# Optimization experiments

Measured on AMD Instinct MI355X. Metric: run time of the kernel, lower is better.

## Reference

```python
import jax, jax.numpy as jnp
import numpy as np

N_NODES = 50000
ALPHA_SLOPE = 0.2  # LeakyReLU negative slope
EPS = 1e-16


def setup_inputs() -> dict:
    key = jax.random.key(0)
    k1, k2, k3, k4 = jax.random.split(key, 4)
    in_features, heads, d = 512, 8, 32
    x = jax.random.normal(k1, (N_NODES, in_features), dtype=jnp.float32)
    edge_index = jax.random.randint(k2, (2, 800000), 0, N_NODES, dtype=jnp.int64)
    # xavier_normal with relu gain ~ sqrt(2) * sqrt(2/(fan_in+fan_out))
    w_std = np.sqrt(2.0) * np.sqrt(2.0 / (in_features + d))
    a_std = np.sqrt(2.0) * np.sqrt(2.0 / (1 + 2 * d))
    W = jax.random.normal(k3, (heads, in_features, d), dtype=jnp.float32) * w_std
    a = jax.random.normal(k4, (heads, 2 * d), dtype=jnp.float32) * a_std
    return {"x": x, "edge_index": edge_index, "W": W, "a": a}


def reference(x, edge_index, W, a):
    # x: [N, F_in], edge_index: [2, E], W: [H, F_in, D], a: [H, 2D]
    n = x.shape[0]
    d = W.shape[-1]
    e0, e1 = edge_index[0], edge_index[1]
    # per-head projected features: [N, H, D]
    h = jnp.einsum('nf,hfd->nhd', x, W)
    # attention logits: a.mm(cat(h[e0], h[e1]).T) == a_src.h[e0] + a_dst.h[e1]
    a_src, a_dst = a[:, :d], a[:, d:]          # [H, D] each
    s_src = jnp.einsum('nhd,hd->nh', h, a_src)  # [N, H]
    s_dst = jnp.einsum('nhd,hd->nh', h, a_dst)  # [N, H]
    logits = s_src[e0] + s_dst[e1]              # [E, H]
    logits = jnp.where(logits >= 0, logits, ALPHA_SLOPE * logits)  # LeakyReLU
    # segment softmax over destination node e0
    m = jax.ops.segment_max(logits, e0, num_segments=n)   # [N, H]
    ex = jnp.exp(logits - m[e0])                          # [E, H]
    denom = jax.ops.segment_sum(ex, e0, num_segments=n)   # [N, H]
    alpha = ex / (denom[e0] + EPS)                        # [E, H]
    # dropout is identity in eval mode
    # sparse aggregate: out[e0] += alpha * h[e1]
    msg = alpha[:, :, None] * h[e1]                       # [E, H, D]
    out = jax.ops.segment_sum(msg, e0, num_segments=n)    # [N, H, D]
    return out.reshape(n, -1)                             # concat heads -> [N, H*D]
```

## Files before the change

### kernel.cpp

```cpp
#include <hip/hip_runtime.h>
#include <hip/hip_bf16.h>

#define N_NODES 50000
#define N_EDGES 800000
#define IN_F    512
#define HEADS   8
#define DHEAD   32
#define NHD     256
#define SLOPE   0.2f
#define EPS_F   1e-16f
#define N_SBLK  ((N_NODES + 255) / 256)
#define NB_GEMM ((N_NODES + 63) / 64)
#define NB_HIST ((N_EDGES + 4095) / 4096)

typedef __attribute__((ext_vector_type(8))) short short8;
typedef __attribute__((ext_vector_type(4))) float f32x4;
typedef __attribute__((ext_vector_type(4))) unsigned short u16x4;
typedef __attribute__((ext_vector_type(4))) unsigned int u32x4;

__device__ __forceinline__ unsigned short f2bf(float f) {
  unsigned int u = __float_as_uint(f);
  unsigned int r = u + 0x7FFFu + ((u >> 16) & 1u);
  return (unsigned short)(r >> 16);
}
__device__ __forceinline__ float bf2f(unsigned short s) {
  return __uint_as_float(((unsigned int)s) << 16);
}
__device__ __forceinline__ unsigned int pkbf(float a, float b) {
  __hip_bfloat162 t = __float22bfloat162_rn(float2{a, b});
  unsigned int r;
  __builtin_memcpy(&r, &t, sizeof(r));
  return r;
}
__device__ __forceinline__ void gload_lds16(const void* g, void* l) {
  __builtin_amdgcn_global_load_lds((const __attribute__((address_space(1))) void*)g,
                                   (__attribute__((address_space(3))) void*)l, 16, 0, 0);
}

__global__ void k_cast_w(const float* __restrict__ W, unsigned short* __restrict__ WbT,
                         int* __restrict__ deg) {
  int id = blockIdx.x * blockDim.x + threadIdx.x;
  if (id < NHD * IN_F) {
    int c = id >> 9, k = id & 511;
    WbT[id] = f2bf(W[(c >> 5) * (IN_F * DHEAD) + k * DHEAD + (c & 31)]);
  }
  if (id < N_NODES) deg[id] = 0;
}

__global__ __launch_bounds__(256) void k_gemm_mfma(const float* __restrict__ x,
                                                   const unsigned short* __restrict__ WbT,
                                                   unsigned short* __restrict__ hb,
                                                   const float* __restrict__ a,
                                                   float* __restrict__ s_src,
                                                   float* __restrict__ s_dst,
                                                   const int* __restrict__ ei,
                                                   int* __restrict__ deg) {
  if (blockIdx.x >= NB_GEMM) {
    int b = blockIdx.x - NB_GEMM;
    int end = min(b * 4096 + 4096, N_EDGES);
    for (int e = b * 4096 + threadIdx.x; e < end; e += 256)
      atomicAdd(&deg[ei[e]], 1);
    return;
  }

  __shared__ unsigned short As[64 * 32];
  __shared__ unsigned short Bs[256 * 32];
  const int tid  = threadIdx.x;
  const int lane = tid & 63;
  const int wid  = tid >> 6;
  const int bm   = blockIdx.x * 64;
  const int wn   = wid * 64;

  const int arow = tid >> 2, ap = tid & 3, aq = ap ^ ((arow >> 1) & 3);
  const float* gA = x + (size_t)min(bm + arow, N_NODES - 1) * IN_F + aq * 8;
  unsigned short* lA = &As[(arow * 4 + ap) * 8];

  const int brow0 = 64 * wid + (lane >> 2);
  const int bq = (lane & 3) ^ ((lane >> 3) & 3);
  const unsigned short* gB0 = WbT + (size_t)brow0 * IN_F + bq * 8;
  unsigned short* lBw = &Bs[((size_t)256 * wid + lane) * 8];

  f32x4 acc[4][4] = {};

#pragma unroll
  for (int t = 0; t < 16; ++t) {
    const int k0 = t * 32;
    __syncthreads();
#pragma unroll
    for (int it = 0; it < 4; ++it)
      gload_lds16(gB0 + k0 + it * 16 * IN_F, lBw + it * 64 * 8);
    {
      float4 lo = *(const float4*)(gA + k0);
      float4 hi = *(const float4*)(gA + k0 + 4);
      u32x4 v = { pkbf(lo.x, lo.y), pkbf(lo.z, lo.w),
                  pkbf(hi.x, hi.y), pkbf(hi.z, hi.w) };
      *(u32x4*)lA = v;
    }
    __syncthreads();

    const int dl = lane & 15;
    const int p  = (lane >> 4) ^ ((dl >> 1) & 3);
    short8 af[4], bfr[4];
#pragma unroll
    for (int i = 0; i < 4; ++i)
      af[i] = *(const short8*)&As[((i * 16 + dl) * 4 + p) * 8];
#pragma unroll
    for (int j = 0; j < 4; ++j)
      bfr[j] = *(const short8*)&Bs[((wn + j * 16 + dl) * 4 + p) * 8];
#pragma unroll
    for (int i = 0; i < 4; ++i)
#pragma unroll
      for (int j = 0; j < 4; ++j)
        acc[i][j] = __builtin_amdgcn_mfma_f32_16x16x32_bf16(af[i], bfr[j], acc[i][j], 0, 0, 0);
  }

  const int h0 = 2 * wid, h1 = 2 * wid + 1;
  const int dl = lane & 15;
  const float as00 = a[h0 * 64 + dl],      as01 = a[h0 * 64 + 16 + dl];
  const float as10 = a[h1 * 64 + dl],      as11 = a[h1 * 64 + 16 + dl];
  const float ad00 = a[h0 * 64 + 32 + dl], ad01 = a[h0 * 64 + 48 + dl];
  const float ad10 = a[h1 * 64 + 32 + dl], ad11 = a[h1 * 64 + 48 + dl];

#pragma unroll
  for (int i = 0; i < 4; ++i) {
#pragma unroll
    for (int q = 0; q < 4; ++q) {
      int row = bm + i * 16 + (lane >> 4) * 4 + q;
      float ss0 = acc[i][0][q] * as00 + acc[i][1][q] * as01;
      float ss1 = acc[i][2][q] * as10 + acc[i][3][q] * as11;
      float sd0 = acc[i][0][q] * ad00 + acc[i][1][q] * ad01;
      float sd1 = acc[i][2][q] * ad10 + acc[i][3][q] * ad11;
#pragma unroll
      for (int o = 1; o < 16; o <<= 1) {
        ss0 += __shfl_xor(ss0, o);
        ss1 += __shfl_xor(ss1, o);
        sd0 += __shfl_xor(sd0, o);
        sd1 += __shfl_xor(sd1, o);
      }
      if (row < N_NODES) {
#pragma unroll
        for (int j = 0; j < 4; ++j)
          hb[(size_t)row * NHD + wn + j * 16 + dl] = f2bf(acc[i][j][q]);
        if (dl == 0) {
          s_src[row * 8 + h0] = ss0;
          s_src[row * 8 + h1] = ss1;
          s_dst[row * 8 + h0] = sd0;
          s_dst[row * 8 + h1] = sd1;
        }
      }
    }
  }
}

__global__ __launch_bounds__(256) void k_bsum(const int* __restrict__ deg,
                                              int* __restrict__ bsum) {
  __shared__ int sm[4];
  int i = blockIdx.x * 256 + threadIdx.x;
  int v = (i < N_NODES) ? deg[i] : 0;
#pragma unroll
  for (int o = 1; o < 64; o <<= 1) v += __shfl_xor(v, o);
  if ((threadIdx.x & 63) == 0) sm[threadIdx.x >> 6] = v;
  __syncthreads();
  if (threadIdx.x == 0) bsum[blockIdx.x] = sm[0] + sm[1] + sm[2] + sm[3];
}

__global__ __launch_bounds__(256) void k_scan_main(const int* __restrict__ deg,
                                                   const int* __restrict__ bsum,
                                                   int* __restrict__ rowptr,
                                                   int* __restrict__ cursor) {
  __shared__ int sb[256];
  __shared__ int sm[256];
  const int t = threadIdx.x;
  const int b = blockIdx.x;
  int bv = (t < N_SBLK) ? bsum[t] : 0;
  sb[t] = bv;
  int i = b * 256 + t;
  int v = (i < N_NODES) ? deg[i] : 0;
  sm[t] = v;
  __syncthreads();
#pragma unroll
  for (int o = 1; o < 256; o <<= 1) {
    int u1 = (t >= o) ? sb[t - o] : 0;
    int u2 = (t >= o) ? sm[t - o] : 0;
    __syncthreads();
    sb[t] += u1;
    sm[t] += u2;
    __syncthreads();
  }
  int boff = (b > 0) ? sb[b - 1] : 0;
  if (i < N_NODES) {
    int ex = boff + sm[t] - v;
    rowptr[i] = ex;
    cursor[i] = ex;
  }
  if (b == 0 && t == 0) rowptr[N_NODES] = sb[255];
}

__global__ void k_fill(const int* __restrict__ ei, int* __restrict__ cursor,
                       int* __restrict__ edst) {
  int e = blockIdx.x * blockDim.x + threadIdx.x;
  if (e >= N_EDGES) return;
  int p = atomicAdd(&cursor[ei[e]], 1);
  edst[p] = ei[N_EDGES + e];
}

__global__ __launch_bounds__(256) void k_aggr(const int* __restrict__ rowptr,
                                              const int* __restrict__ edst,
                                              const float* __restrict__ s_src,
                                              const float* __restrict__ s_dst,
                                              const unsigned short* __restrict__ hb,
                                              float* __restrict__ out) {
  int n = (int)((blockIdx.x * blockDim.x + threadIdx.x) >> 6);
  if (n >= N_NODES) return;
  n = __builtin_amdgcn_readfirstlane(n);
  const int lane = threadIdx.x & 63;
  const int head = lane >> 3;
  const float ssrc = s_src[n * 8 + head];
  int i = rowptr[n];
  const int iend = rowptr[n + 1];
  float den = 0.f;
  f32x4 acc = {0.f, 0.f, 0.f, 0.f};
  for (; i + 1 < iend; i += 2) {
    int d0 = edst[i], d1 = edst[i + 1];
    float v0 = ssrc + s_dst[d0 * 8 + head];
    float v1 = ssrc + s_dst[d1 * 8 + head];
    u16x4 h0 = *(const u16x4*)(hb + (size_t)d0 * NHD + lane * 4);
    u16x4 h1 = *(const u16x4*)(hb + (size_t)d1 * NHD + lane * 4);
    v0 = v0 >= 0.f ? v0 : SLOPE * v0;
    v1 = v1 >= 0.f ? v1 : SLOPE * v1;
    float e0 = __expf(v0), e1 = __expf(v1);
    den += e0 + e1;
    acc.x += e0 * bf2f(h0.x) + e1 * bf2f(h1.x);
    acc.y += e0 * bf2f(h0.y) + e1 * bf2f(h1.y);
    acc.z += e0 * bf2f(h0.z) + e1 * bf2f(h1.z);
    acc.w += e0 * bf2f(h0.w) + e1 * bf2f(h1.w);
  }
  if (i < iend) {
    int d0 = edst[i];
    float v0 = ssrc + s_dst[d0 * 8 + head];
    v0 = v0 >= 0.f ? v0 : SLOPE * v0;
    float e0 = __expf(v0);
    u16x4 h0 = *(const u16x4*)(hb + (size_t)d0 * NHD + lane * 4);
    den += e0;
    acc.x += e0 * bf2f(h0.x);
    acc.y += e0 * bf2f(h0.y);
    acc.z += e0 * bf2f(h0.z);
    acc.w += e0 * bf2f(h0.w);
  }
  float inv = 1.f / (den + EPS_F);
  *(f32x4*)(out + (size_t)n * NHD + lane * 4) = acc * inv;
}

extern "C" void kernel_launch(void* const* d_in, const int* in_sizes, int n_in,
                              void* d_out, int out_size, void* d_ws, size_t ws_size,
                              hipStream_t stream) {
  const float* x  = (const float*)d_in[0];
  const int*   ei = (const int*)d_in[1];
  const float* W  = (const float*)d_in[2];
  const float* a  = (const float*)d_in[3];
  float* out = (float*)d_out;

  unsigned short* hb  = (unsigned short*)d_ws;
  unsigned short* WbT = hb + (size_t)N_NODES * NHD;
  float* s_src = (float*)(WbT + (size_t)NHD * IN_F);
  float* s_dst = s_src + (size_t)N_NODES * HEADS;
  int* deg    = (int*)(s_dst + (size_t)N_NODES * HEADS);
  int* cursor = deg + N_NODES;
  int* rowptr = cursor + N_NODES;
  int* bsum   = rowptr + 50008;
  int* edst   = bsum + 256;

  k_cast_w<<<512, 256, 0, stream>>>(W, WbT, deg);
  k_gemm_mfma<<<NB_GEMM + NB_HIST, 256, 0, stream>>>(x, WbT, hb, a, s_src, s_dst, ei, deg);
  k_bsum<<<N_SBLK, 256, 0, stream>>>(deg, bsum);
  k_scan_main<<<N_SBLK, 256, 0, stream>>>(deg, bsum, rowptr, cursor);
  k_fill<<<(N_EDGES + 255) / 256, 256, 0, stream>>>(ei, cursor, edst);
  k_aggr<<<(N_NODES * 64 + 255) / 256, 256, 0, stream>>>(rowptr, edst, s_src, s_dst, hb, out);
}
```

Measured before the change: 184.3 us.

## Pre-cast x to bf16 in output buffer and retile GEMM to 128x128 blocks

```diff
diff --git a/kernel.cpp b/kernel.cpp
--- a/kernel.cpp
+++ b/kernel.cpp
@@ -10,8 +10,10 @@
 #define SLOPE   0.2f
 #define EPS_F   1e-16f
 #define N_SBLK  ((N_NODES + 255) / 256)
-#define NB_GEMM ((N_NODES + 63) / 64)
+#define NB_M    ((N_NODES + 127) / 128)
+#define NB_GEMM (NB_M * 2)
 #define NB_HIST ((N_EDGES + 4095) / 4096)
+#define NB_XCST ((N_NODES * IN_F / 8 + 255) / 256)
 
 typedef __attribute__((ext_vector_type(8))) short short8;
 typedef __attribute__((ext_vector_type(4))) float f32x4;
@@ -37,17 +39,30 @@
                                    (__attribute__((address_space(3))) void*)l, 16, 0, 0);
 }
 
-__global__ void k_cast_w(const float* __restrict__ W, unsigned short* __restrict__ WbT,
-                         int* __restrict__ deg) {
-  int id = blockIdx.x * blockDim.x + threadIdx.x;
-  if (id < NHD * IN_F) {
-    int c = id >> 9, k = id & 511;
-    WbT[id] = f2bf(W[(c >> 5) * (IN_F * DHEAD) + k * DHEAD + (c & 31)]);
-  }
-  if (id < N_NODES) deg[id] = 0;
-}
-
-__global__ __launch_bounds__(256) void k_gemm_mfma(const float* __restrict__ x,
+__global__ __launch_bounds__(256) void k_prep(const float* __restrict__ x,
+                                              unsigned short* __restrict__ xb,
+                                              const float* __restrict__ W,
+                                              unsigned short* __restrict__ WbT,
+                                              int* __restrict__ deg) {
+  int b = blockIdx.x;
+  if (b < NB_XCST) {
+    size_t id = (size_t)b * 256 + threadIdx.x;
+    const float4* src = (const float4*)(x + id * 8);
+    float4 lo = src[0], hi = src[1];
+    u32x4 v = { pkbf(lo.x, lo.y), pkbf(lo.z, lo.w),
+                pkbf(hi.x, hi.y), pkbf(hi.z, hi.w) };
+    *(u32x4*)(xb + id * 8) = v;
+  } else {
+    int id = (b - NB_XCST) * 256 + threadIdx.x;
+    if (id < NHD * IN_F) {
+      int c = id >> 9, k = id & 511;
+      WbT[id] = f2bf(W[(c >> 5) * (IN_F * DHEAD) + k * DHEAD + (c & 31)]);
+    }
+    if (id < N_NODES) deg[id] = 0;
+  }
+}
+
+__global__ __launch_bounds__(256) void k_gemm_mfma(const unsigned short* __restrict__ xb,
                                                    const unsigned short* __restrict__ WbT,
                                                    unsigned short* __restrict__ hb,
                                                    const float* __restrict__ a,
@@ -63,59 +78,57 @@
     return;
   }
 
-  __shared__ unsigned short As[64 * 32];
-  __shared__ unsigned short Bs[256 * 32];
+  __shared__ unsigned short As[128 * 64];
+  __shared__ unsigned short Bs[128 * 64];
   const int tid  = threadIdx.x;
   const int lane = tid & 63;
   const int wid  = tid >> 6;
-  const int bm   = blockIdx.x * 64;
-  const int wn   = wid * 64;
-
-  const int arow = tid >> 2, ap = tid & 3, aq = ap ^ ((arow >> 1) & 3);
-  const float* gA = x + (size_t)min(bm + arow, N_NODES - 1) * IN_F + aq * 8;
-  unsigned short* lA = &As[(arow * 4 + ap) * 8];
-
-  const int brow0 = 64 * wid + (lane >> 2);
-  const int bq = (lane & 3) ^ ((lane >> 3) & 3);
-  const unsigned short* gB0 = WbT + (size_t)brow0 * IN_F + bq * 8;
-  unsigned short* lBw = &Bs[((size_t)256 * wid + lane) * 8];
+  const int wr   = wid >> 1;
+  const int wc   = wid & 1;
+  const int bm   = (blockIdx.x >> 1) * 128;
+  const int bn   = (blockIdx.x & 1) * 128;
+
+  const int rl0 = 32 * wid + (lane >> 3);
+  const int qq  = lane & 7;
+  const unsigned short* gA = xb + (size_t)min(bm + rl0, N_NODES - 1) * IN_F + qq * 8;
+  const unsigned short* gB = WbT + (size_t)(bn + rl0) * IN_F + qq * 8;
+  unsigned short* lA = &As[(size_t)(32 * wid) * 64 + lane * 8];
+  unsigned short* lB = &Bs[(size_t)(32 * wid) * 64 + lane * 8];
 
   f32x4 acc[4][4] = {};
-
-#pragma unroll
-  for (int t = 0; t < 16; ++t) {
-    const int k0 = t * 32;
-    __syncthreads();
-#pragma unroll
-    for (int it = 0; it < 4; ++it)
-      gload_lds16(gB0 + k0 + it * 16 * IN_F, lBw + it * 64 * 8);
-    {
-      float4 lo = *(const float4*)(gA + k0);
-      float4 hi = *(const float4*)(gA + k0 + 4);
-      u32x4 v = { pkbf(lo.x, lo.y), pkbf(lo.z, lo.w),
-                  pkbf(hi.x, hi.y), pkbf(hi.z, hi.w) };
-      *(u32x4*)lA = v;
-    }
-    __syncthreads();
-
-    const int dl = lane & 15;
-    const int p  = (lane >> 4) ^ ((dl >> 1) & 3);
-    short8 af[4], bfr[4];
-#pragma unroll
-    for (int i = 0; i < 4; ++i)
-      af[i] = *(const short8*)&As[((i * 16 + dl) * 4 + p) * 8];
-#pragma unroll
-    for (int j = 0; j < 4; ++j)
-      bfr[j] = *(const short8*)&Bs[((wn + j * 16 + dl) * 4 + p) * 8];
-#pragma unroll
-    for (int i = 0; i < 4; ++i)
+  const int dl = lane & 15;
+  const int qg = lane >> 4;
+
+#pragma unroll
+  for (int t = 0; t < 8; ++t) {
+    const int k0 = t * 64;
+    __syncthreads();
+#pragma unroll
+    for (int it = 0; it < 4; ++it) {
+      gload_lds16(gA + k0 + (size_t)it * 8 * IN_F, lA + it * 8 * 64);
+      gload_lds16(gB + k0 + (size_t)it * 8 * IN_F, lB + it * 8 * 64);
+    }
+    __syncthreads();
+
+#pragma unroll
+    for (int kk = 0; kk < 2; ++kk) {
+      short8 af[4], bfr[4];
+#pragma unroll
+      for (int i = 0; i < 4; ++i)
+        af[i] = *(const short8*)&As[(wr * 64 + i * 16 + dl) * 64 + kk * 32 + qg * 8];
 #pragma unroll
       for (int j = 0; j < 4; ++j)
-        acc[i][j] = __builtin_amdgcn_mfma_f32_16x16x32_bf16(af[i], bfr[j], acc[i][j], 0, 0, 0);
-  }
-
-  const int h0 = 2 * wid, h1 = 2 * wid + 1;
-  const int dl = lane & 15;
+        bfr[j] = *(const short8*)&Bs[(wc * 64 + j * 16 + dl) * 64 + kk * 32 + qg * 8];
+#pragma unroll
+      for (int i = 0; i < 4; ++i)
+#pragma unroll
+        for (int j = 0; j < 4; ++j)
+          acc[i][j] = __builtin_amdgcn_mfma_f32_16x16x32_bf16(af[i], bfr[j], acc[i][j], 0, 0, 0);
+    }
+  }
+
+  const int cb = bn + wc * 64;
+  const int h0 = cb >> 5, h1 = h0 + 1;
   const float as00 = a[h0 * 64 + dl],      as01 = a[h0 * 64 + 16 + dl];
   const float as10 = a[h1 * 64 + dl],      as11 = a[h1 * 64 + 16 + dl];
   const float ad00 = a[h0 * 64 + 32 + dl], ad01 = a[h0 * 64 + 48 + dl];
@@ -125,7 +138,7 @@
   for (int i = 0; i < 4; ++i) {
 #pragma unroll
     for (int q = 0; q < 4; ++q) {
-      int row = bm + i * 16 + (lane >> 4) * 4 + q;
+      int row = bm + wr * 64 + i * 16 + qg * 4 + q;
       float ss0 = acc[i][0][q] * as00 + acc[i][1][q] * as01;
       float ss1 = acc[i][2][q] * as10 + acc[i][3][q] * as11;
       float sd0 = acc[i][0][q] * ad00 + acc[i][1][q] * ad01;
@@ -140,7 +153,7 @@
       if (row < N_NODES) {
 #pragma unroll
         for (int j = 0; j < 4; ++j)
-          hb[(size_t)row * NHD + wn + j * 16 + dl] = f2bf(acc[i][j][q]);
+          hb[(size_t)row * NHD + cb + j * 16 + dl] = f2bf(acc[i][j][q]);
         if (dl == 0) {
           s_src[row * 8 + h0] = ss0;
           s_src[row * 8 + h1] = ss1;
@@ -259,6 +272,7 @@
   const float* W  = (const float*)d_in[2];
   const float* a  = (const float*)d_in[3];
   float* out = (float*)d_out;
+  unsigned short* xb = (unsigned short*)d_out;
 
   unsigned short* hb  = (unsigned short*)d_ws;
   unsigned short* WbT = hb + (size_t)N_NODES * NHD;
@@ -270,8 +284,8 @@
   int* bsum   = rowptr + 50008;
   int* edst   = bsum + 256;
 
-  k_cast_w<<<512, 256, 0, stream>>>(W, WbT, deg);
-  k_gemm_mfma<<<NB_GEMM + NB_HIST, 256, 0, stream>>>(x, WbT, hb, a, s_src, s_dst, ei, deg);
+  k_prep<<<NB_XCST + 512, 256, 0, stream>>>(x, xb, W, WbT, deg);
+  k_gemm_mfma<<<NB_GEMM + NB_HIST, 256, 0, stream>>>(xb, WbT, hb, a, s_src, s_dst, ei, deg);
   k_bsum<<<N_SBLK, 256, 0, stream>>>(deg, bsum);
   k_scan_main<<<N_SBLK, 256, 0, stream>>>(deg, bsum, rowptr, cursor);
   k_fill<<<(N_EDGES + 255) / 256, 256, 0, stream>>>(ei, cursor, edst);
```

Result: slower. 210.1 us (+14.0%).
